# Performance work log

Measured on AMD Instinct MI355X. Metric: run time of the kernel, lower is better.

Reference implementation:

```python
import jax, jax.numpy as jnp
import numpy as np
from jax import lax

B, T, L = 256, 512, 128


def setup_inputs() -> dict:
    key = jax.random.key(0)
    k1, k2, k3 = jax.random.split(key, 3)
    labels = jax.random.randint(k1, (B, T), 0, L)
    y_true = jax.nn.one_hot(labels, L, dtype=jnp.float32)  # [B,T,L]
    y_pred = jax.random.normal(k2, (B, T, L), dtype=jnp.float32)
    trans = jax.random.normal(k3, (L, L), dtype=jnp.float32) * 0.1
    return {"y_true": y_true, "y_pred": y_pred, "trans": trans}


def reference(y_true, y_pred, trans):
    # ---- log partition via forward algorithm (lax.scan over time) ----
    init = y_pred[:, 0]  # [B,L] initial alpha

    def step(alpha, emit):  # alpha [B,L], emit [B,L]
        # alpha[:, i, None] + trans[i, j] -> logsumexp over previous label i
        new = jax.nn.logsumexp(alpha[:, :, None] + trans[None, :, :], axis=1) + emit
        return new, None

    emits = jnp.swapaxes(y_pred[:, 1:], 0, 1)  # [T-1,B,L]
    final_alpha, _ = lax.scan(step, init, emits)  # [B,L]
    log_norm = jax.nn.logsumexp(final_alpha, axis=1, keepdims=True)  # [B,1]

    # ---- path score (unnormalized log prob of the true path) ----
    point_score = jnp.sum(y_pred * y_true, axis=(1, 2), keepdims=False)[:, None]  # [B,1]
    trans_score = jnp.einsum('bti,btj,ij->b', y_true[:, :-1], y_true[:, 1:], trans)[:, None]  # [B,1]

    return log_norm - (point_score + trans_score)  # [B,1]
```

## Files before the change

### kernel.cpp

```cpp
#include <hip/hip_runtime.h>

typedef float  f32x4 __attribute__((ext_vector_type(4)));
typedef short  s16x8 __attribute__((ext_vector_type(8)));

#define Tt 512
#define Ll 128
#define CH 16
#define CL 32
#define NR 15
#define RUNS 30
#define NSCORE 256

#define WS_PT 0
#define WS_TR 256
#define WS_KR 512
#define WS_KB (512 + 256*NR)
#define WS_RV (512 + 2*256*NR)
#define WS_BV (WS_RV + 256*NR*128)

__device__ __forceinline__ void bar_lgkm() {
  asm volatile("s_waitcnt lgkmcnt(0)" ::: "memory");
  __builtin_amdgcn_s_barrier();
  asm volatile("" ::: "memory");
}
__device__ __forceinline__ ushort bf16rn(float f) {
  unsigned u = __float_as_uint(f);
  u += 0x7FFFu + ((u >> 16) & 1u);
  return (ushort)(u >> 16);
}
__device__ __forceinline__ float bf16tof(ushort h) {
  return __uint_as_float(((unsigned)h) << 16);
}

__global__ __launch_bounds__(512, 1) void crf_chunk(
    const float* __restrict__ yt_g, const float* __restrict__ yp_g,
    const float* __restrict__ tr_g, float* __restrict__ wsf)
{
  __shared__ __align__(16) ushort ubuf[2][16 * 128];
  __shared__ int   lab_s[Tt];
  __shared__ float redp[8], redt[8];

  const int tid = threadIdx.x, wv = tid >> 6, l = tid & 63;

  if (blockIdx.x < NSCORE) {
    const int b = blockIdx.x;
    const float4* yp4 = (const float4*)(yp_g + (size_t)b * Tt * Ll);
    const float4* yt4 = (const float4*)(yt_g + (size_t)b * Tt * Ll);
    float pt = 0.f;
    #pragma unroll 4
    for (int i = 0; i < 32; ++i) {
      int f = tid + i * 512;
      float4 a = yp4[f], y = yt4[f];
      pt += a.x * y.x + a.y * y.y + a.z * y.z + a.w * y.w;
      int t = f >> 5, jb = (f & 31) << 2;
      if (y.x > .5f) lab_s[t] = jb;
      if (y.y > .5f) lab_s[t] = jb + 1;
      if (y.z > .5f) lab_s[t] = jb + 2;
      if (y.w > .5f) lab_s[t] = jb + 3;
    }
    __syncthreads();
    float trl = (tid < Tt - 1) ? tr_g[lab_s[tid] * Ll + lab_s[tid + 1]] : 0.f;
    #pragma unroll
    for (int o = 32; o; o >>= 1) { pt += __shfl_xor(pt, o); trl += __shfl_xor(trl, o); }
    if (l == 0) { redp[wv] = pt; redt[wv] = trl; }
    __syncthreads();
    if (tid == 0) {
      float sp = 0.f, st = 0.f;
      #pragma unroll
      for (int k2 = 0; k2 < 8; ++k2) { sp += redp[k2]; st += redt[k2]; }
      wsf[WS_PT + b] = sp; wsf[WS_TR + b] = st;
    }
    return;
  }

  const int bid2 = blockIdx.x - NSCORE;
  const int g    = bid2 / RUNS, run = bid2 % RUNS;
  const bool FWD = (run < NR);
  const int c    = FWD ? run : (run - NR + 1);
  const int b0   = g * 16;
  const int l15  = l & 15, q = l >> 4;
  const int jg   = (wv << 4) | l15;
  const int swA  = (l15 & 7) << 4;

  const int t_hi = (c == CH - 1) ? (Tt - 1) : (c * CL + CL);
  const int t_lo = c * CL + 1;
  const int n    = FWD ? CL : (t_hi - t_lo + 1);

  s16x8 Bf[4];
  #pragma unroll
  for (int kt = 0; kt < 4; ++kt) {
    s16x8 v;
    #pragma unroll
    for (int e = 0; e < 8; ++e) {
      int k = 32 * kt + 8 * q + e;
      float tv = FWD ? tr_g[k * Ll + l15] : tr_g[l15 * Ll + k];
      v[e] = (short)bf16rn(__expf(tv));
    }
    Bf[kt] = v;
  }

  const size_t ypb0 = ((size_t)(b0 + 4 * q + 0) * Tt) * Ll + jg;
  const size_t ypb1 = ((size_t)(b0 + 4 * q + 1) * Tt) * Ll + jg;
  const size_t ypb2 = ((size_t)(b0 + 4 * q + 2) * Tt) * Ll + jg;
  const size_t ypb3 = ((size_t)(b0 + 4 * q + 3) * Tt) * Ll + jg;

  float K0 = 0.f, K1 = 0.f, K2 = 0.f, K3 = 0.f;
  float res0 = 0.f, res1 = 0.f, res2 = 0.f, res3 = 0.f;

  {
    float iv0, iv1, iv2, iv3;
    if (FWD) {
      if (c == 0) {
        iv0 = __expf(yp_g[ypb0]); iv1 = __expf(yp_g[ypb1]);
        iv2 = __expf(yp_g[ypb2]); iv3 = __expf(yp_g[ypb3]);
      } else { iv0 = iv1 = iv2 = iv3 = 1.f; }
    } else {
      size_t off = (size_t)t_hi * Ll;
      iv0 = __expf(yp_g[ypb0 + off]); iv1 = __expf(yp_g[ypb1 + off]);
      iv2 = __expf(yp_g[ypb2 + off]); iv3 = __expf(yp_g[ypb3 + off]);
    }
    char* wb = (char*)ubuf;
    *(ushort*)(wb + (4*q+0)*256 + ((2*jg) ^ (((4*q+0)&7)<<4))) = bf16rn(iv0);
    *(ushort*)(wb + (4*q+1)*256 + ((2*jg) ^ (((4*q+1)&7)<<4))) = bf16rn(iv1);
    *(ushort*)(wb + (4*q+2)*256 + ((2*jg) ^ (((4*q+2)&7)<<4))) = bf16rn(iv2);
    *(ushort*)(wb + (4*q+3)*256 + ((2*jg) ^ (((4*q+3)&7)<<4))) = bf16rn(iv3);
  }

  float PEa0, PEa1, PEa2, PEa3, PEb0, PEb1, PEb2, PEb3;
  {
    size_t o0 = (size_t)(FWD ? t_lo : (t_hi - 1)) * Ll;
    PEa0 = yp_g[ypb0+o0]; PEa1 = yp_g[ypb1+o0]; PEa2 = yp_g[ypb2+o0]; PEa3 = yp_g[ypb3+o0];
    size_t o1 = (size_t)(FWD ? (t_lo + 1) : (t_hi - 2)) * Ll;
    PEb0 = yp_g[ypb0+o1]; PEb1 = yp_g[ypb1+o1]; PEb2 = yp_g[ypb2+o1]; PEb3 = yp_g[ypb3+o1];
  }
  bar_lgkm();

#define ITER(K_, PE0,PE1,PE2,PE3)                                             \
  {                                                                           \
    const int cur = (K_) & 1;                                                 \
    const char* abase = (const char*)ubuf + cur * 4096 + l15 * 256;           \
    f32x4 dd = {0.f, 0.f, 0.f, 0.f};                                          \
    _Pragma("unroll")                                                         \
    for (int kt = 0; kt < 4; ++kt) {                                          \
      float4 af = *(const float4*)(abase + ((64 * kt + 16 * q) ^ swA));       \
      dd = __builtin_amdgcn_mfma_f32_16x16x32_bf16(*(const s16x8*)&af,        \
             Bf[kt], dd, 0, 0, 0);                                            \
    }                                                                         \
    const bool last = (K_) == n - 1;                                          \
    const bool ren  = (((K_) & 7) == 7);                                      \
    float wex0 = __expf(PE0), wex1 = __expf(PE1),                             \
          wex2 = __expf(PE2), wex3 = __expf(PE3);                             \
    float rn0 = 1.f, rn1 = 1.f, rn2 = 1.f, rn3 = 1.f;                         \
    if (ren) {                                                                \
      const char* pb = (const char*)ubuf + cur * 4096;                        \
      float p0 = bf16tof(*(const ushort*)(pb + (4*q+0)*256 + (((4*q+0)&7)<<4))); \
      float p1 = bf16tof(*(const ushort*)(pb + (4*q+1)*256 + (((4*q+1)&7)<<4))); \
      float p2 = bf16tof(*(const ushort*)(pb + (4*q+2)*256 + (((4*q+2)&7)<<4))); \
      float p3 = bf16tof(*(const ushort*)(pb + (4*q+3)*256 + (((4*q+3)&7)<<4))); \
      K0 += __logf(p0); K1 += __logf(p1); K2 += __logf(p2); K3 += __logf(p3); \
      rn0 = 1.f / p0; rn1 = 1.f / p1; rn2 = 1.f / p2; rn3 = 1.f / p3;         \
    }                                                                         \
    float v0 = dd[0], v1 = dd[1], v2 = dd[2], v3 = dd[3];                     \
    if (!(!FWD && last)) { v0 *= wex0; v1 *= wex1; v2 *= wex2; v3 *= wex3; }  \
    if (ren) { v0 *= rn0; v1 *= rn1; v2 *= rn2; v3 *= rn3; }                  \
    if (last) { res0 = v0; res1 = v1; res2 = v2; res3 = v3; }                 \
    else {                                                                    \
      char* wb = (char*)ubuf + (cur ^ 1) * 4096;                              \
      *(ushort*)(wb + (4*q+0)*256 + ((2*jg) ^ (((4*q+0)&7)<<4))) = bf16rn(v0);\
      *(ushort*)(wb + (4*q+1)*256 + ((2*jg) ^ (((4*q+1)&7)<<4))) = bf16rn(v1);\
      *(ushort*)(wb + (4*q+2)*256 + ((2*jg) ^ (((4*q+2)&7)<<4))) = bf16rn(v2);\
      *(ushort*)(wb + (4*q+3)*256 + ((2*jg) ^ (((4*q+3)&7)<<4))) = bf16rn(v3);\
    }                                                                         \
    if ((K_) + 2 < n) {                                                       \
      const size_t o2 = (size_t)(FWD ? (t_lo + (K_) + 2)                      \
                                     : (t_hi - (K_) - 3)) * Ll;               \
      PE0 = yp_g[ypb0+o2]; PE1 = yp_g[ypb1+o2];                               \
      PE2 = yp_g[ypb2+o2]; PE3 = yp_g[ypb3+o2];                               \
    }                                                                         \
    bar_lgkm();                                                               \
  }

  for (int k = 0; k < n; k += 2) {
    ITER(k, PEa0, PEa1, PEa2, PEa3)
    if (k + 1 < n) {
      ITER(k + 1, PEb0, PEb1, PEb2, PEb3)
    }
  }
#undef ITER

  {
    const int cs = FWD ? c : (c - 1);
    float* rp = wsf + (FWD ? WS_RV : WS_BV);
    rp[((size_t)(b0 + 4*q + 0) * NR + cs) * 128 + jg] = res0;
    rp[((size_t)(b0 + 4*q + 1) * NR + cs) * 128 + jg] = res1;
    rp[((size_t)(b0 + 4*q + 2) * NR + cs) * 128 + jg] = res2;
    rp[((size_t)(b0 + 4*q + 3) * NR + cs) * 128 + jg] = res3;
    if (wv == 0 && l15 == 0) {
      float* kp = wsf + (FWD ? WS_KR : WS_KB);
      kp[(b0 + 4*q + 0) * NR + cs] = K0;
      kp[(b0 + 4*q + 1) * NR + cs] = K1;
      kp[(b0 + 4*q + 2) * NR + cs] = K2;
      kp[(b0 + 4*q + 3) * NR + cs] = K3;
    }
  }
}

__global__ __launch_bounds__(64) void crf_stitch(
    const float* __restrict__ wsf, float* __restrict__ out)
{
  const int b = blockIdx.x, j = threadIdx.x;
  const float* RV = wsf + WS_RV + (size_t)b * NR * 128;
  const float* BV = wsf + WS_BV + (size_t)b * NR * 128;
  const float* Kr = wsf + WS_KR + b * NR;
  const float* Kb = wsf + WS_KB + b * NR;
  float lz;
  {
    float d = RV[j] * BV[j] + RV[j + 64] * BV[j + 64];
    #pragma unroll
    for (int o = 32; o; o >>= 1) d += __shfl_xor(d, o);
    lz = __logf(d) + Kr[0] + Kb[0];
  }
  #pragma unroll
  for (int cc = 1; cc < NR; ++cc) {
    float d = RV[cc*128 + j] * BV[cc*128 + j] + RV[cc*128 + j + 64] * BV[cc*128 + j + 64];
    float s = RV[cc*128 + j] + RV[cc*128 + j + 64];
    #pragma unroll
    for (int o = 32; o; o >>= 1) { d += __shfl_xor(d, o); s += __shfl_xor(s, o); }
    lz += __logf(d) - __logf(s) + Kb[cc];
  }
  if (j == 0) out[b] = lz - wsf[WS_PT + b] - wsf[WS_TR + b];
}

extern "C" void kernel_launch(void* const* d_in, const int* in_sizes, int n_in,
                              void* d_out, int out_size, void* d_ws, size_t ws_size,
                              hipStream_t stream) {
  const float* y_true = (const float*)d_in[0];
  const float* y_pred = (const float*)d_in[1];
  const float* trans  = (const float*)d_in[2];
  float* out = (float*)d_out;
  float* wsf = (float*)d_ws;
  crf_chunk<<<dim3(NSCORE + 16 * RUNS), dim3(512), 0, stream>>>(y_true, y_pred, trans, wsf);
  crf_stitch<<<dim3(256), dim3(64), 0, stream>>>(wsf, out);
}
```

Baseline: 65.79 us.

## Restructure CRF chunk recursion into per-wave tasks with transpose LDS reads

```diff
diff --git a/kernel.cpp b/kernel.cpp
--- a/kernel.cpp
+++ b/kernel.cpp
@@ -1,14 +1,16 @@
 #include <hip/hip_runtime.h>
 
-typedef float  f32x4 __attribute__((ext_vector_type(4)));
-typedef short  s16x8 __attribute__((ext_vector_type(8)));
+typedef float    f32x4  __attribute__((ext_vector_type(4)));
+typedef short    s16x8  __attribute__((ext_vector_type(8)));
+typedef unsigned uivec2 __attribute__((ext_vector_type(2)));
+typedef unsigned uivec4 __attribute__((ext_vector_type(4)));
 
 #define Tt 512
 #define Ll 128
-#define CH 16
-#define CL 32
-#define NR 15
-#define RUNS 30
+#define CH 32
+#define CL 16
+#define NR 31
+#define NRECB 248
 #define NSCORE 256
 
 #define WS_PT 0
@@ -18,38 +20,48 @@
 #define WS_RV (512 + 2*256*NR)
 #define WS_BV (WS_RV + 256*NR*128)
 
-__device__ __forceinline__ void bar_lgkm() {
-  asm volatile("s_waitcnt lgkmcnt(0)" ::: "memory");
-  __builtin_amdgcn_s_barrier();
-  asm volatile("" ::: "memory");
-}
 __device__ __forceinline__ ushort bf16rn(float f) {
   unsigned u = __float_as_uint(f);
   u += 0x7FFFu + ((u >> 16) & 1u);
   return (ushort)(u >> 16);
 }
-__device__ __forceinline__ float bf16tof(ushort h) {
-  return __uint_as_float(((unsigned)h) << 16);
-}
-
-__global__ __launch_bounds__(512, 1) void crf_chunk(
-    const float* __restrict__ yt_g, const float* __restrict__ yp_g,
-    const float* __restrict__ tr_g, float* __restrict__ wsf)
+__device__ __forceinline__ unsigned cvtpk(float a, float b) {
+  unsigned d;
+  asm("v_cvt_pk_bf16_f32 %0, %1, %2" : "=v"(d) : "v"(a), "v"(b));
+  return d;
+}
+__device__ __forceinline__ float4 expf4(float4 v) {
+  float4 r; r.x = __expf(v.x); r.y = __expf(v.y); r.z = __expf(v.z); r.w = __expf(v.w);
+  return r;
+}
+__device__ __forceinline__ float4 mul4(float4 v, float s) {
+  v.x *= s; v.y *= s; v.z *= s; v.w *= s; return v;
+}
+
+__global__ __attribute__((amdgpu_flat_work_group_size(256, 256),
+                          amdgpu_waves_per_eu(1)))
+void crf_main(const float* __restrict__ yt_g, const float* __restrict__ yp_g,
+              const float* __restrict__ tr_g, float* __restrict__ wsf)
 {
-  __shared__ __align__(16) ushort ubuf[2][16 * 128];
-  __shared__ int   lab_s[Tt];
-  __shared__ float redp[8], redt[8];
-
+  __shared__ __align__(16) char smem[32768];
   const int tid = threadIdx.x, wv = tid >> 6, l = tid & 63;
-
-  if (blockIdx.x < NSCORE) {
-    const int b = blockIdx.x;
+  const int bid = blockIdx.x;
+
+  bool isrec; int sidx = 0, ridx = 0;
+  if (bid < 2 * NRECB) { isrec = (bid & 1); sidx = ridx = bid >> 1; }
+  else { isrec = false; sidx = NRECB + (bid - 2 * NRECB); }
+
+  if (!isrec) {
+    int*   lab_s = (int*)smem;
+    float* redp  = (float*)(smem + 2048);
+    float* redt  = (float*)(smem + 2080);
+    const int b = sidx;
     const float4* yp4 = (const float4*)(yp_g + (size_t)b * Tt * Ll);
     const float4* yt4 = (const float4*)(yt_g + (size_t)b * Tt * Ll);
     float pt = 0.f;
     #pragma unroll 4
-    for (int i = 0; i < 32; ++i) {
-      int f = tid + i * 512;
+    for (int i = 0; i < 64; ++i) {
+      int f = tid + i * 256;
       float4 a = yp4[f], y = yt4[f];
       pt += a.x * y.x + a.y * y.y + a.z * y.z + a.w * y.w;
       int t = f >> 5, jb = (f & 31) << 2;
@@ -59,150 +71,223 @@
       if (y.w > .5f) lab_s[t] = jb + 3;
     }
     __syncthreads();
-    float trl = (tid < Tt - 1) ? tr_g[lab_s[tid] * Ll + lab_s[tid + 1]] : 0.f;
+    float trl = 0.f;
+    for (int t0 = tid; t0 < Tt - 1; t0 += 256)
+      trl += tr_g[lab_s[t0] * Ll + lab_s[t0 + 1]];
     #pragma unroll
     for (int o = 32; o; o >>= 1) { pt += __shfl_xor(pt, o); trl += __shfl_xor(trl, o); }
     if (l == 0) { redp[wv] = pt; redt[wv] = trl; }
     __syncthreads();
     if (tid == 0) {
-      float sp = 0.f, st = 0.f;
-      #pragma unroll
-      for (int k2 = 0; k2 < 8; ++k2) { sp += redp[k2]; st += redt[k2]; }
-      wsf[WS_PT + b] = sp; wsf[WS_TR + b] = st;
+      wsf[WS_PT + b] = redp[0] + redp[1] + redp[2] + redp[3];
+      wsf[WS_TR + b] = redt[0] + redt[1] + redt[2] + redt[3];
     }
     return;
   }
 
-  const int bid2 = blockIdx.x - NSCORE;
-  const int g    = bid2 / RUNS, run = bid2 % RUNS;
-  const bool FWD = (run < NR);
-  const int c    = FWD ? run : (run - NR + 1);
-  const int b0   = g * 16;
-  const int l15  = l & 15, q = l >> 4;
-  const int jg   = (wv << 4) | l15;
-  const int swA  = (l15 & 7) << 4;
-
+  const int task = ridx * 4 + wv;
+  const bool FWD = task < 496;
+  int g, c;
+  if (FWD) { g = task / 31; c = task % 31; }
+  else     { int t2 = task - 496; g = t2 / 31; c = t2 % 31 + 1; }
+  const int b0  = g * 16;
+  const int l15 = l & 15, q = l >> 4;
   const int t_hi = (c == CH - 1) ? (Tt - 1) : (c * CL + CL);
   const int t_lo = c * CL + 1;
   const int n    = FWD ? CL : (t_hi - t_lo + 1);
 
-  s16x8 Bf[4];
-  #pragma unroll
-  for (int kt = 0; kt < 4; ++kt) {
-    s16x8 v;
-    #pragma unroll
-    for (int e = 0; e < 8; ++e) {
-      int k = 32 * kt + 8 * q + e;
-      float tv = FWD ? tr_g[k * Ll + l15] : tr_g[l15 * Ll + k];
-      v[e] = (short)bf16rn(__expf(tv));
-    }
-    Bf[kt] = v;
-  }
-
-  const size_t ypb0 = ((size_t)(b0 + 4 * q + 0) * Tt) * Ll + jg;
-  const size_t ypb1 = ((size_t)(b0 + 4 * q + 1) * Tt) * Ll + jg;
-  const size_t ypb2 = ((size_t)(b0 + 4 * q + 2) * Tt) * Ll + jg;
-  const size_t ypb3 = ((size_t)(b0 + 4 * q + 3) * Tt) * Ll + jg;
-
-  float K0 = 0.f, K1 = 0.f, K2 = 0.f, K3 = 0.f;
-  float res0 = 0.f, res1 = 0.f, res2 = 0.f, res3 = 0.f;
+  s16x8 Bf[8][4];
+  if (FWD) {
+    #pragma unroll
+    for (int kt = 0; kt < 4; ++kt)
+      #pragma unroll
+      for (int e = 0; e < 8; ++e) {
+        const int jin = 32 * kt + 16 * (e >> 2) + 4 * q + (e & 3);
+        const float* rp_ = tr_g + jin * Ll + l15;
+        #pragma unroll
+        for (int tl = 0; tl < 8; ++tl)
+          Bf[tl][kt][e] = (short)bf16rn(__expf(rp_[16 * tl]));
+      }
+  } else {
+    #pragma unroll
+    for (int tl = 0; tl < 8; ++tl) {
+      const float* rp_ = tr_g + (l15 + 16 * tl) * Ll + 4 * q;
+      #pragma unroll
+      for (int kt = 0; kt < 4; ++kt)
+        #pragma unroll
+        for (int r = 0; r < 2; ++r) {
+          float4 tv = *(const float4*)(rp_ + 32 * kt + 16 * r);
+          Bf[tl][kt][4 * r + 0] = (short)bf16rn(__expf(tv.x));
+          Bf[tl][kt][4 * r + 1] = (short)bf16rn(__expf(tv.y));
+          Bf[tl][kt][4 * r + 2] = (short)bf16rn(__expf(tv.z));
+          Bf[tl][kt][4 * r + 3] = (short)bf16rn(__expf(tv.w));
+        }
+    }
+  }
+
+  const unsigned sbase = (unsigned)(size_t)(&smem[0]);
+  const unsigned wvoff = (unsigned)(wv * 8192);
+  const unsigned lane8 = (unsigned)(l * 8);
+  const int wroff = wv * 8192 + l15 * 32 + q * 8;
+  const float* emb = yp_g + (size_t)(b0 + l15) * (Tt * Ll) + 4 * q;
+  float Kacc = 0.f;
+
+#define LOADSLOT(S, TAU)                                                      \
+  { const float* ep_ = emb + (size_t)(TAU) * Ll;                              \
+    S##0 = *(const float4*)(ep_ + 0);   S##1 = *(const float4*)(ep_ + 16);    \
+    S##2 = *(const float4*)(ep_ + 32);  S##3 = *(const float4*)(ep_ + 48);    \
+    S##4 = *(const float4*)(ep_ + 64);  S##5 = *(const float4*)(ep_ + 80);    \
+    S##6 = *(const float4*)(ep_ + 96);  S##7 = *(const float4*)(ep_ + 112); }
+
+#define TRREAD8(RBUF, T0,T1,T2,T3,T4,T5,T6,T7)                                \
+  { unsigned ra_ = sbase + wvoff + (unsigned)((RBUF) * 4096) + lane8;         \
+    asm volatile(                                                             \
+      "ds_read_b64_tr_b16 %0, %8 offset:0\n\t"                                \
+      "ds_read_b64_tr_b16 %1, %8 offset:512\n\t"                              \
+      "ds_read_b64_tr_b16 %2, %8 offset:1024\n\t"                             \
+      "ds_read_b64_tr_b16 %3, %8 offset:1536\n\t"                             \
+      "ds_read_b64_tr_b16 %4, %8 offset:2048\n\t"                             \
+      "ds_read_b64_tr_b16 %5, %8 offset:2560\n\t"                             \
+      "ds_read_b64_tr_b16 %6, %8 offset:3072\n\t"                             \
+      "ds_read_b64_tr_b16 %7, %8 offset:3584\n\t"                             \
+      "s_waitcnt lgkmcnt(0)"                                                  \
+      : "=v"(T0), "=v"(T1), "=v"(T2), "=v"(T3),                               \
+        "=v"(T4), "=v"(T5), "=v"(T6), "=v"(T7)                                \
+      : "v"(ra_) : "memory"); }
+
+#define BUILDA(A_, TA, TB, WA, WB_)                                           \
+  { uivec4 au_;                                                               \
+    au_.x = cvtpk(__uint_as_float(TA.x << 16) * WA.x,                         \
+                  __uint_as_float(TA.x & 0xFFFF0000u) * WA.y);                \
+    au_.y = cvtpk(__uint_as_float(TA.y << 16) * WA.z,                         \
+                  __uint_as_float(TA.y & 0xFFFF0000u) * WA.w);                \
+    au_.z = cvtpk(__uint_as_float(TB.x << 16) * WB_.x,                        \
+                  __uint_as_float(TB.x & 0xFFFF0000u) * WB_.y);               \
+    au_.w = cvtpk(__uint_as_float(TB.y << 16) * WB_.z,                        \
+                  __uint_as_float(TB.y & 0xFFFF0000u) * WB_.w);               \
+    A_ = __builtin_bit_cast(s16x8, au_); }
+
+#define MFMAW(WBUF)                                                           \
+  { f32x4 dd[8];                                                              \
+    _Pragma("unroll")                                                         \
+    for (int tl = 0; tl < 8; ++tl) {                                          \
+      f32x4 z = {0.f, 0.f, 0.f, 0.f};                                         \
+      z = __builtin_amdgcn_mfma_f32_16x16x32_bf16(A0, Bf[tl][0], z, 0, 0, 0); \
+      z = __builtin_amdgcn_mfma_f32_16x16x32_bf16(A1, Bf[tl][1], z, 0, 0, 0); \
+      z = __builtin_amdgcn_mfma_f32_16x16x32_bf16(A2, Bf[tl][2], z, 0, 0, 0); \
+      z = __builtin_amdgcn_mfma_f32_16x16x32_bf16(A3, Bf[tl][3], z, 0, 0, 0); \
+      dd[tl] = z;                                                             \
+    }                                                                         \
+    _Pragma("unroll")                                                         \
+    for (int tl = 0; tl < 8; ++tl) {                                          \
+      uivec2 w_;                                                              \
+      w_.x = cvtpk(dd[tl][0], dd[tl][1]);                                     \
+      w_.y = cvtpk(dd[tl][2], dd[tl][3]);                                     \
+      *(uivec2*)(smem + wroff + (WBUF) * 4096 + tl * 512) = w_;               \
+    } }
+
+#define MULT(RBUF, WBUF, S, REN, PT, PSLOT)                                   \
+  { asm volatile("s_waitcnt lgkmcnt(0)" ::: "memory");                        \
+    uivec2 t0, t1, t2, t3, t4, t5, t6, t7;                                    \
+    TRREAD8(RBUF, t0, t1, t2, t3, t4, t5, t6, t7)                             \
+    float4 we0 = expf4(S##0), we1 = expf4(S##1), we2 = expf4(S##2),           \
+           we3 = expf4(S##3), we4 = expf4(S##4), we5 = expf4(S##5),           \
+           we6 = expf4(S##6), we7 = expf4(S##7);                              \
+    if (REN) {                                                                \
+      float pf = __uint_as_float(__builtin_amdgcn_readfirstlane(t0.x << 16)); \
+      Kacc += __logf(pf);                                                     \
+      float rs = __builtin_amdgcn_rcpf(pf);                                   \
+      we0 = mul4(we0, rs); we1 = mul4(we1, rs); we2 = mul4(we2, rs);          \
+      we3 = mul4(we3, rs); we4 = mul4(we4, rs); we5 = mul4(we5, rs);          \
+      we6 = mul4(we6, rs); we7 = mul4(we7, rs);                               \
+    }                                                                         \
+    s16x8 A0, A1, A2, A3;                                                     \
+    BUILDA(A0, t0, t1, we0, we1)                                              \
+    BUILDA(A1, t2, t3, we2, we3)                                              \
+    BUILDA(A2, t4, t5, we4, we5)                                              \
+    BUILDA(A3, t6, t7, we6, we7)                                              \
+    MFMAW(WBUF)                                                               \
+    if ((PT) >= 0) LOADSLOT(PSLOT, PT) }
+
+  float4 SA0, SA1, SA2, SA3, SA4, SA5, SA6, SA7;
+  float4 SB0, SB1, SB2, SB3, SB4, SB5, SB6, SB7;
+  const int tau1 = FWD ? (t_lo - 1) : t_hi;
+  const int tau2 = FWD ? t_lo : (t_hi - 1);
+  LOADSLOT(SB, tau1)
+  LOADSLOT(SA, tau2)
 
   {
-    float iv0, iv1, iv2, iv3;
+    s16x8 A0, A1, A2, A3;
+    if (FWD && c > 0) {
+      uivec4 au; au.x = au.y = au.z = au.w = 0x3F803F80u;
+      A0 = __builtin_bit_cast(s16x8, au); A1 = A0; A2 = A0; A3 = A0;
+    } else {
+      float4 we0 = expf4(SB0), we1 = expf4(SB1), we2 = expf4(SB2),
+             we3 = expf4(SB3), we4 = expf4(SB4), we5 = expf4(SB5),
+             we6 = expf4(SB6), we7 = expf4(SB7);
+      uivec4 a0; a0.x = cvtpk(we0.x, we0.y); a0.y = cvtpk(we0.z, we0.w);
+      a0.z = cvtpk(we1.x, we1.y); a0.w = cvtpk(we1.z, we1.w);
+      uivec4 a1; a1.x = cvtpk(we2.x, we2.y); a1.y = cvtpk(we2.z, we2.w);
+      a1.z = cvtpk(we3.x, we3.y); a1.w = cvtpk(we3.z, we3.w);
+      uivec4 a2; a2.x = cvtpk(we4.x, we4.y); a2.y = cvtpk(we4.z, we4.w);
+      a2.z = cvtpk(we5.x, we5.y); a2.w = cvtpk(we5.z, we5.w);
+      uivec4 a3; a3.x = cvtpk(we6.x, we6.y); a3.y = cvtpk(we6.z, we6.w);
+      a3.z = cvtpk(we7.x, we7.y); a3.w = cvtpk(we7.z, we7.w);
+      A0 = __builtin_bit_cast(s16x8, a0); A1 = __builtin_bit_cast(s16x8, a1);
+      A2 = __builtin_bit_cast(s16x8, a2); A3 = __builtin_bit_cast(s16x8, a3);
+    }
+    MFMAW(1)
+    const int tau3 = FWD ? (t_lo + 1) : (t_hi - 2);
+    LOADSLOT(SB, tau3)
+  }
+
+  for (int k = 2; k + 1 <= n; k += 2) {
+    const int ta = FWD ? (t_lo + k) : (t_hi - k - 1);
+    MULT(1, 0, SA, false, ta, SA)
+    const bool ren = ((k + 1) == 9) || ((k + 1) == 15);
+    const int tb = (k + 3 <= n + 1) ? (FWD ? (t_lo + k + 1) : (t_hi - k - 2))
+                                    : -1;
+    MULT(0, 1, SB, ren, tb, SB)
+  }
+  if ((n & 1) == 0) {
+    MULT(1, 0, SA, false, -1, SA)
+  }
+
+  {
+    asm volatile("s_waitcnt lgkmcnt(0)" ::: "memory");
+    uivec2 t0, t1, t2, t3, t4, t5, t6, t7;
+    TRREAD8((n & 1), t0, t1, t2, t3, t4, t5, t6, t7)
+    float4 wf0, wf1, wf2, wf3, wf4, wf5, wf6, wf7;
     if (FWD) {
-      if (c == 0) {
-        iv0 = __expf(yp_g[ypb0]); iv1 = __expf(yp_g[ypb1]);
-        iv2 = __expf(yp_g[ypb2]); iv3 = __expf(yp_g[ypb3]);
-      } else { iv0 = iv1 = iv2 = iv3 = 1.f; }
+      wf0 = expf4(SB0); wf1 = expf4(SB1); wf2 = expf4(SB2); wf3 = expf4(SB3);
+      wf4 = expf4(SB4); wf5 = expf4(SB5); wf6 = expf4(SB6); wf7 = expf4(SB7);
     } else {
-      size_t off = (size_t)t_hi * Ll;
-      iv0 = __expf(yp_g[ypb0 + off]); iv1 = __expf(yp_g[ypb1 + off]);
-      iv2 = __expf(yp_g[ypb2 + off]); iv3 = __expf(yp_g[ypb3 + off]);
-    }
-    char* wb = (char*)ubuf;
-    *(ushort*)(wb + (4*q+0)*256 + ((2*jg) ^ (((4*q+0)&7)<<4))) = bf16rn(iv0);
-    *(ushort*)(wb + (4*q+1)*256 + ((2*jg) ^ (((4*q+1)&7)<<4))) = bf16rn(iv1);
-    *(ushort*)(wb + (4*q+2)*256 + ((2*jg) ^ (((4*q+2)&7)<<4))) = bf16rn(iv2);
-    *(ushort*)(wb + (4*q+3)*256 + ((2*jg) ^ (((4*q+3)&7)<<4))) = bf16rn(iv3);
-  }
-
-  float PEa0, PEa1, PEa2, PEa3, PEb0, PEb1, PEb2, PEb3;
-  {
-    size_t o0 = (size_t)(FWD ? t_lo : (t_hi - 1)) * Ll;
-    PEa0 = yp_g[ypb0+o0]; PEa1 = yp_g[ypb1+o0]; PEa2 = yp_g[ypb2+o0]; PEa3 = yp_g[ypb3+o0];
-    size_t o1 = (size_t)(FWD ? (t_lo + 1) : (t_hi - 2)) * Ll;
-    PEb0 = yp_g[ypb0+o1]; PEb1 = yp_g[ypb1+o1]; PEb2 = yp_g[ypb2+o1]; PEb3 = yp_g[ypb3+o1];
-  }
-  bar_lgkm();
-
-#define ITER(K_, PE0,PE1,PE2,PE3)                                             \
-  {                                                                           \
-    const int cur = (K_) & 1;                                                 \
-    const char* abase = (const char*)ubuf + cur * 4096 + l15 * 256;           \
-    f32x4 dd = {0.f, 0.f, 0.f, 0.f};                                          \
-    _Pragma("unroll")                                                         \
-    for (int kt = 0; kt < 4; ++kt) {                                          \
-      float4 af = *(const float4*)(abase + ((64 * kt + 16 * q) ^ swA));       \
-      dd = __builtin_amdgcn_mfma_f32_16x16x32_bf16(*(const s16x8*)&af,        \
-             Bf[kt], dd, 0, 0, 0);                                            \
-    }                                                                         \
-    const bool last = (K_) == n - 1;                                          \
-    const bool ren  = (((K_) & 7) == 7);                                      \
-    float wex0 = __expf(PE0), wex1 = __expf(PE1),                             \
-          wex2 = __expf(PE2), wex3 = __expf(PE3);                             \
-    float rn0 = 1.f, rn1 = 1.f, rn2 = 1.f, rn3 = 1.f;                         \
-    if (ren) {                                                                \
-      const char* pb = (const char*)ubuf + cur * 4096;                        \
-      float p0 = bf16tof(*(const ushort*)(pb + (4*q+0)*256 + (((4*q+0)&7)<<4))); \
-      float p1 = bf16tof(*(const ushort*)(pb + (4*q+1)*256 + (((4*q+1)&7)<<4))); \
-      float p2 = bf16tof(*(const ushort*)(pb + (4*q+2)*256 + (((4*q+2)&7)<<4))); \
-      float p3 = bf16tof(*(const ushort*)(pb + (4*q+3)*256 + (((4*q+3)&7)<<4))); \
-      K0 += __logf(p0); K1 += __logf(p1); K2 += __logf(p2); K3 += __logf(p3); \
-      rn0 = 1.f / p0; rn1 = 1.f / p1; rn2 = 1.f / p2; rn3 = 1.f / p3;         \
-    }                                                                         \
-    float v0 = dd[0], v1 = dd[1], v2 = dd[2], v3 = dd[3];                     \
-    if (!(!FWD && last)) { v0 *= wex0; v1 *= wex1; v2 *= wex2; v3 *= wex3; }  \
-    if (ren) { v0 *= rn0; v1 *= rn1; v2 *= rn2; v3 *= rn3; }                  \
-    if (last) { res0 = v0; res1 = v1; res2 = v2; res3 = v3; }                 \
-    else {                                                                    \
-      char* wb = (char*)ubuf + (cur ^ 1) * 4096;                              \
-      *(ushort*)(wb + (4*q+0)*256 + ((2*jg) ^ (((4*q+0)&7)<<4))) = bf16rn(v0);\
-      *(ushort*)(wb + (4*q+1)*256 + ((2*jg) ^ (((4*q+1)&7)<<4))) = bf16rn(v1);\
-      *(ushort*)(wb + (4*q+2)*256 + ((2*jg) ^ (((4*q+2)&7)<<4))) = bf16rn(v2);\
-      *(ushort*)(wb + (4*q+3)*256 + ((2*jg) ^ (((4*q+3)&7)<<4))) = bf16rn(v3);\
-    }                                                                         \
-    if ((K_) + 2 < n) {                                                       \
-      const size_t o2 = (size_t)(FWD ? (t_lo + (K_) + 2)                      \
-                                     : (t_hi - (K_) - 3)) * Ll;               \
-      PE0 = yp_g[ypb0+o2]; PE1 = yp_g[ypb1+o2];                               \
-      PE2 = yp_g[ypb2+o2]; PE3 = yp_g[ypb3+o2];                               \
-    }                                                                         \
-    bar_lgkm();                                                               \
-  }
-
-  for (int k = 0; k < n; k += 2) {
-    ITER(k, PEa0, PEa1, PEa2, PEa3)
-    if (k + 1 < n) {
-      ITER(k + 1, PEb0, PEb1, PEb2, PEb3)
-    }
-  }
-#undef ITER
-
-  {
+      float4 one = {1.f, 1.f, 1.f, 1.f};
+      wf0 = wf1 = wf2 = wf3 = wf4 = wf5 = wf6 = wf7 = one;
+    }
     const int cs = FWD ? c : (c - 1);
-    float* rp = wsf + (FWD ? WS_RV : WS_BV);
-    rp[((size_t)(b0 + 4*q + 0) * NR + cs) * 128 + jg] = res0;
-    rp[((size_t)(b0 + 4*q + 1) * NR + cs) * 128 + jg] = res1;
-    rp[((size_t)(b0 + 4*q + 2) * NR + cs) * 128 + jg] = res2;
-    rp[((size_t)(b0 + 4*q + 3) * NR + cs) * 128 + jg] = res3;
-    if (wv == 0 && l15 == 0) {
+    float* rp0 = wsf + (FWD ? WS_RV : WS_BV)
+               + ((size_t)(b0 + l15) * NR + cs) * 128 + 4 * q;
+#define STOREV(I, T_, W_)                                                     \
+    { float4 o_;                                                              \
+      o_.x = __uint_as_float(T_.x << 16) * W_.x;                              \
+      o_.y = __uint_as_float(T_.x & 0xFFFF0000u) * W_.y;                      \
+      o_.z = __uint_as_float(T_.y << 16) * W_.z;                              \
+      o_.w = __uint_as_float(T_.y & 0xFFFF0000u) * W_.w;                      \
+      *(float4*)(rp0 + 16 * (I)) = o_; }
+    STOREV(0, t0, wf0) STOREV(1, t1, wf1) STOREV(2, t2, wf2) STOREV(3, t3, wf3)
+    STOREV(4, t4, wf4) STOREV(5, t5, wf5) STOREV(6, t6, wf6) STOREV(7, t7, wf7)
+#undef STOREV
+    if (q == 0) {
       float* kp = wsf + (FWD ? WS_KR : WS_KB);
-      kp[(b0 + 4*q + 0) * NR + cs] = K0;
-      kp[(b0 + 4*q + 1) * NR + cs] = K1;
-      kp[(b0 + 4*q + 2) * NR + cs] = K2;
-      kp[(b0 + 4*q + 3) * NR + cs] = K3;
-    }
-  }
+      kp[(b0 + l15) * NR + cs] = Kacc;
+    }
+  }
+#undef MULT
+#undef MFMAW
+#undef BUILDA
+#undef TRREAD8
+#undef LOADSLOT
 }
 
 __global__ __launch_bounds__(64) void crf_stitch(
@@ -239,6 +324,7 @@
   const float* trans  = (const float*)d_in[2];
   float* out = (float*)d_out;
   float* wsf = (float*)d_ws;
-  crf_chunk<<<dim3(NSCORE + 16 * RUNS), dim3(512), 0, stream>>>(y_true, y_pred, trans, wsf);
+  crf_main<<<dim3(2 * NRECB + (NSCORE - NRECB)), dim3(256), 0, stream>>>(
+      y_true, y_pred, trans, wsf);
   crf_stitch<<<dim3(256), dim3(64), 0, stream>>>(wsf, out);
 }
```

After: 70.92 us. +7.8%, slower.
